# Kernel optimization log

Hardware: AMD Instinct MI355X
Metric: run time of the kernel (lower is better)

Reference implementation:

```python
import jax, jax.numpy as jnp
import numpy as np

B, L, H, E = 16, 4096, 8, 64
K = 64  # topk modes
SCALE = 1.0 / (512 * 512)  # 1/(in_channels*out_channels)


def setup_inputs() -> dict:
    key = jax.random.key(0)
    k1, k2, k3 = jax.random.split(key, 3)
    q = jax.random.normal(k1, (B, L, H, E), dtype=jnp.float32)
    k = jnp.zeros((B, L, H, E), jnp.float32)  # unused by module
    v = jnp.zeros((B, L, H, E), jnp.float32)  # unused by module
    mask = jnp.zeros((1,), jnp.int32)         # unused by module
    w_real = jax.random.uniform(k2, (K, H, E, E), dtype=jnp.float32) * SCALE
    w_imag = jax.random.uniform(k3, (K, H, E, E), dtype=jnp.float32) * SCALE
    return {"q": q, "k": k, "v": v, "w_real": w_real, "w_imag": w_imag, "mask": mask}


def reference(q, k, v, w_real, w_imag, mask):
    # x_ft: (B, F, H, Ein) complex64, F = L//2 + 1
    x_ft = jnp.fft.rfft(q.astype(jnp.float32), axis=1)
    F = x_ft.shape[1]
    kk = w_real.shape[0]
    # energy score per bin: sum |.|^2 over Ein, mean over batch, mean over heads
    e = (x_ft.real ** 2 + x_ft.imag ** 2).sum(-1)      # (B, F, H)
    score = e.mean(0).mean(-1)                          # (F,)
    score = score.at[0].set(-jnp.inf)                   # topk_exclude_dc=True
    _, idx = jax.lax.top_k(score, kk)                   # sorted desc by energy
    # gather selected modes: (B, K, H, Ein)
    x_sel = x_ft[:, idx]
    w = jax.lax.complex(w_real, w_imag)                 # (K, H, Ein, Eout)
    out_sel = jnp.einsum('bkhe,khef->bkhf', x_sel, w)   # per-head complex matmul
    # packed scatter: selected modes written into the first K bins of zero spectrum
    out_ft = jnp.zeros((x_ft.shape[0], F, x_ft.shape[2], w.shape[-1]), jnp.complex64)
    out_ft = out_ft.at[:, :kk].set(out_sel)
    # inverse FFT back to time domain, norm='backward' (default)
    return jnp.fft.irfft(out_ft, n=q.shape[1], axis=1)
```

## Files before the change

### kernel.cpp

```cpp
#include <hip/hip_runtime.h>


#define NTHREADS 256

__device__ inline void lds_barrier() {
    asm volatile("s_waitcnt lgkmcnt(0)" ::: "memory");
    __builtin_amdgcn_s_barrier();
}

#define ZI(i) ((i) ^ ((((i) >> 4) & 7) << 1))

__device__ inline float2 f2add(float2 a, float2 b) { return make_float2(a.x + b.x, a.y + b.y); }
__device__ inline float2 f2sub(float2 a, float2 b) { return make_float2(a.x - b.x, a.y - b.y); }
__device__ inline float2 cmulf(float2 a, float2 b) {
    return make_float2(__builtin_fmaf(a.x, b.x, -(a.y * b.y)),
                       __builtin_fmaf(a.x, b.y,  a.y * b.x));
}

__device__ inline void radix16(float2 x[16], float2 tA, float2 tB, float2 tC, float2 tD) {
#pragma unroll
    for (int q = 0; q < 8; ++q) {
        float2 v = cmulf(tA, x[2 * q + 1]);
        float2 u = x[2 * q];
        x[2 * q]     = f2add(u, v);
        x[2 * q + 1] = f2sub(u, v);
    }
    {
        float2 tB1 = make_float2(tB.y, -tB.x);
#pragma unroll
        for (int q = 0; q < 4; ++q) {
            {
                float2 v = cmulf(tB, x[4 * q + 2]);
                float2 u = x[4 * q];
                x[4 * q]     = f2add(u, v);
                x[4 * q + 2] = f2sub(u, v);
            }
            {
                float2 v = cmulf(tB1, x[4 * q + 3]);
                float2 u = x[4 * q + 1];
                x[4 * q + 1] = f2add(u, v);
                x[4 * q + 3] = f2sub(u, v);
            }
        }
    }
    {
        const float C = 0.70710678118654752f;
        float2 w0 = tC;
        float2 w1 = cmulf(tC, make_float2(C, -C));
        float2 w2 = make_float2(tC.y, -tC.x);
        float2 w3 = cmulf(tC, make_float2(-C, -C));
#pragma unroll
        for (int q = 0; q < 2; ++q) {
            float2 ws[4] = {w0, w1, w2, w3};
#pragma unroll
            for (int r = 0; r < 4; ++r) {
                float2 v = cmulf(ws[r], x[8 * q + r + 4]);
                float2 u = x[8 * q + r];
                x[8 * q + r]     = f2add(u, v);
                x[8 * q + r + 4] = f2sub(u, v);
            }
        }
    }
    {
        const float C  = 0.70710678118654752f;
        const float C1 = 0.92387953251128676f;
        const float S1 = 0.38268343236508977f;
        float2 wD[8];
        wD[0] = tD;
        wD[1] = cmulf(tD, make_float2(C1, -S1));
        wD[2] = cmulf(tD, make_float2(C, -C));
        wD[3] = cmulf(tD, make_float2(S1, -C1));
        wD[4] = make_float2(tD.y, -tD.x);
        wD[5] = cmulf(tD, make_float2(-S1, -C1));
        wD[6] = cmulf(tD, make_float2(-C, -C));
        wD[7] = cmulf(tD, make_float2(-C1, -S1));
#pragma unroll
        for (int r = 0; r < 8; ++r) {
            float2 v = cmulf(wD[r], x[r + 8]);
            float2 u = x[r];
            x[r]     = f2add(u, v);
            x[r + 8] = f2sub(u, v);
        }
    }
}

__global__ void k_tables(float2* __restrict__ trig, unsigned long long* __restrict__ score) {
    int k = blockIdx.x * blockDim.x + threadIdx.x;
    if (k < 4096) {
        double th = (6.283185307179586476925286766559 * (double)k) / 4096.0;
        trig[k] = make_float2((float)cos(th), (float)sin(th));
    }
    if (k < 2048) score[k] = 0ULL;
}

__global__ __launch_bounds__(256) void k_xpose(const float* __restrict__ q,
                                               float2* __restrict__ T) {
    __shared__ float tile[128][65];

    const int tid = threadIdx.x;
    const int bi  = blockIdx.x;
    const int b   = bi >> 8;
    const int h   = (bi >> 5) & 7;
    const int c5  = bi & 31;

    const float* qb = q + ((size_t)b * 4096 * 512) + (size_t)h * 64;
#pragma unroll
    for (int i = 0; i < 8; ++i) {
        const int f = tid + 256 * i;
        const int t = f >> 4, e4 = f & 15;
        const float4 v = *(const float4*)(qb + (size_t)(c5 + 32 * t) * 512 + e4 * 4);
        tile[t][e4 * 4 + 0] = v.x;
        tile[t][e4 * 4 + 1] = v.y;
        tile[t][e4 * 4 + 2] = v.z;
        tile[t][e4 * 4 + 3] = v.w;
    }
    lds_barrier();

    const int wave = tid >> 6, lane = tid & 63;
    const int rl  = __brev(lane) >> 26;
    const int r5c = __brev(c5) >> 27;
    for (int cc = wave; cc < 32; cc += 4) {
        const int eo = cc >> 2, p = cc & 3;
        const int col0 = eo * 8 + 2 * p;
        float2* dst = T + ((size_t)((b * 8 + h) * 8 + eo)) * 16384 + (size_t)p * 4096
                        + (size_t)r5c * 128;
        float4 o;
        o.x = tile[rl][col0];      o.y = tile[rl][col0 + 1];
        o.z = tile[rl + 64][col0]; o.w = tile[rl + 64][col0 + 1];
        *(float4*)(dst + 2 * lane) = o;
    }
}

__global__ __launch_bounds__(256) void k_fft(const float2* __restrict__ trig,
                                             float2* __restrict__ Xout,
                                             unsigned long long* __restrict__ score) {
    __shared__ float2 z[4096];
    __shared__ float2 ctw4[80];

    const int tid = threadIdx.x;
    const int bi  = blockIdx.x;

    if (tid < 64) {
        const int j = tid >> 2, qq = tid & 3;
        float2 a = trig[j << (7 - qq)];
        ctw4[5 * j + qq] = make_float2(a.x, -a.y);
    }

    float eaccr[8];
#pragma unroll
    for (int k = 0; k < 8; ++k) eaccr[k] = 0.f;

    const float2 ONE = make_float2(1.0f, 0.0f);
    const float2* base = Xout + (size_t)bi * 16384;

    float4 pre[8];
#pragma unroll
    for (int g = 0; g < 8; ++g) pre[g] = *(const float4*)(base + 16 * tid + 2 * g);
    lds_barrier();

    for (int p = 0; p < 4; ++p) {
        float2 x[16];
#pragma unroll
        for (int g = 0; g < 8; ++g) {
            x[2 * g]     = make_float2(pre[g].x, pre[g].y);
            x[2 * g + 1] = make_float2(pre[g].z, pre[g].w);
        }
        if (p < 3) {
            const float2* pn = base + (size_t)(p + 1) * 4096;
#pragma unroll
            for (int g = 0; g < 8; ++g) pre[g] = *(const float4*)(pn + 16 * tid + 2 * g);
        }

        radix16(x, ONE, ONE, ONE, ONE);
        {
            const int i0 = 16 * tid;
#pragma unroll
            for (int s = 0; s < 8; ++s) {
                *(float4*)&z[ZI(i0 + 2 * s)] = make_float4(x[2 * s].x, x[2 * s].y,
                                                           x[2 * s + 1].x, x[2 * s + 1].y);
            }
        }
        lds_barrier();

        {
            const int j = tid & 15;
            const int g = tid >> 4;
            const int i0 = (g << 8) + j;
            int ad[16];
#pragma unroll
            for (int k = 0; k < 16; ++k) ad[k] = ZI(i0 + 16 * k);
#pragma unroll
            for (int k = 0; k < 16; ++k) x[k] = z[ad[k]];
            const float2 tA = ctw4[5 * j + 0];
            const float2 tB = ctw4[5 * j + 1];
            const float2 tC = ctw4[5 * j + 2];
            const float2 tD = ctw4[5 * j + 3];
            radix16(x, tA, tB, tC, tD);
#pragma unroll
            for (int k = 0; k < 16; ++k) z[ad[k]] = x[k];
        }
        lds_barrier();

        {
            const int j = tid;
            int ad[16];
#pragma unroll
            for (int k = 0; k < 16; ++k) ad[k] = ZI(j + 256 * k);
#pragma unroll
            for (int k = 0; k < 16; ++k) x[k] = z[ad[k]];
            float2 a = trig[j << 3], b2 = trig[j << 2], c = trig[j << 1], d = trig[j];
            const float2 tA = make_float2(a.x, -a.y);
            const float2 tB = make_float2(b2.x, -b2.y);
            const float2 tC = make_float2(c.x, -c.y);
            const float2 tD = make_float2(d.x, -d.y);
            radix16(x, tA, tB, tC, tD);
#pragma unroll
            for (int k = 0; k < 16; ++k) z[ad[k]] = x[k];
        }
        lds_barrier();

        {
            const size_t s0 = (size_t)bi * 16384 + (size_t)p * 4096;
#pragma unroll
            for (int k = 0; k < 8; ++k) {
                const int t = tid + 256 * k;
                const int m = t + 1;
                float2 Za = z[ZI(m)];
                float2 Zb = z[ZI(4096 - m)];
                float Xr0 = 0.5f * (Za.x + Zb.x);
                float Xi0 = 0.5f * (Za.y - Zb.y);
                float Xr1 = 0.5f * (Za.y + Zb.y);
                float Xi1 = 0.5f * (Zb.x - Za.x);
                Xout[s0 + t]        = make_float2(Xr0, Xi0);
                Xout[s0 + 2048 + t] = make_float2(Xr1, Xi1);
                eaccr[k] += Xr0 * Xr0 + Xi0 * Xi0 + Xr1 * Xr1 + Xi1 * Xi1;
            }
        }
        lds_barrier();
    }

#pragma unroll
    for (int k = 0; k < 8; ++k) {
        unsigned long long v = (unsigned long long)llrintf(eaccr[k] * 1048576.0f);
        atomicAdd(&score[tid + 256 * k], v);
    }
}

__global__ __launch_bounds__(256) void k_topk(const unsigned long long* __restrict__ score,
                                              int* __restrict__ idx) {
    __shared__ unsigned long long s[2048];
    const int tid = threadIdx.x;
    for (int t = tid; t < 2048; t += 256) s[t] = score[t];
    __syncthreads();

    const int t = blockIdx.x * 256 + tid;
    const unsigned long long my = s[t];
    int rank = 0;
#pragma unroll 8
    for (int u = 0; u < 2048; ++u) {
        unsigned long long o = s[u];
        rank += (int)((o > my) || (o == my && u < t));
    }
    if (rank < 64) idx[rank] = t + 1;
}

__global__ __launch_bounds__(256) void k_proj(const float2* __restrict__ X,
                                              const float* __restrict__ wr,
                                              const float* __restrict__ wi,
                                              const int* __restrict__ idx,
                                              float2* __restrict__ Y) {
    __shared__ __align__(16) float2 xs[4 * 64];
    __shared__ float  wrs[64 * 64];
    __shared__ float  wis[64 * 64];

    const int tid = threadIdx.x;
    const int j  = blockIdx.x >> 5;
    const int h  = (blockIdx.x >> 2) & 7;
    const int bq = blockIdx.x & 3;
    const int m = idx[j];

    {
        const int bl = tid >> 6, e = tid & 63;
        xs[tid] = X[((size_t)(((bq * 4 + bl) * 8 + h) * 64 + e)) * 2048 + (size_t)(m - 1)];
    }
    const float* wrb = wr + ((size_t)(j * 8 + h)) * 4096;
    const float* wib = wi + ((size_t)(j * 8 + h)) * 4096;
#pragma unroll
    for (int i = 0; i < 16; ++i) {
        const int t = tid + 256 * i;
        wrs[t] = wrb[t];
        wis[t] = wib[t];
    }
    lds_barrier();

    const int bl = tid >> 6;
    const int f  = tid & 63;
    const float2* xrow = &xs[bl * 64];
    float yr = 0.f, yi = 0.f;
#pragma unroll
    for (int e = 0; e < 64; e += 4) {
        const float4 xa = *(const float4*)&xrow[e];
        const float4 xb = *(const float4*)&xrow[e + 2];
        const float2 xv[4] = {make_float2(xa.x, xa.y), make_float2(xa.z, xa.w),
                              make_float2(xb.x, xb.y), make_float2(xb.z, xb.w)};
#pragma unroll
        for (int d = 0; d < 4; ++d) {
            const float a = wrs[(e + d) * 64 + f], cc = wis[(e + d) * 64 + f];
            yr = __builtin_fmaf(xv[d].x, a, yr); yr = __builtin_fmaf(-xv[d].y, cc, yr);
            yi = __builtin_fmaf(xv[d].x, cc, yi); yi = __builtin_fmaf( xv[d].y, a, yi);
        }
    }
    const int b = bq * 4 + bl;
    Y[((size_t)b * 64 + j) * 512 + (size_t)(h * 64 + f)] = make_float2(yr, yi);
}

__global__ __launch_bounds__(256, 4) void k_synth(const float2* __restrict__ Y,
                                                  const float2* __restrict__ trig,
                                                  float* __restrict__ out) {
    __shared__ __align__(16) float2 ys[64][32];

    const int tid = threadIdx.x;
    const int bi  = blockIdx.x;
    const int b   = bi >> 8;
    const int hft = (bi >> 4) & 15;
    const int lt  = bi & 15;

    const float invN = 1.0f / 4096.0f;
    const float2* yb = Y + (size_t)b * 64 * 512 + (size_t)hft * 32;
    for (int t = tid; t < 64 * 32; t += NTHREADS) {
        int j = t >> 5, cc = t & 31;
        float2 y = yb[(size_t)j * 512 + cc];
        if (j == 0) ys[0][cc] = make_float2(y.x * invN, 0.0f);
        else        ys[j][cc] = make_float2(y.x * (2.0f * invN), y.y * (2.0f * invN));
    }
    lds_barrier();

    const int r = tid >> 3;
    const int c = tid & 7;
    const int l0 = lt * 64 + r * 2;

    float2 rot[2], w[2];
#pragma unroll
    for (int v = 0; v < 2; ++v) {
        w[v] = trig[(l0 + v) & 4095];
        rot[v] = make_float2(1.0f, 0.0f);
    }

    float F0[2][4], F1[2][4], F2[2][4], F3[2][4], H1[2][4], H3[2][4];
#pragma unroll
    for (int v = 0; v < 2; ++v)
#pragma unroll
        for (int u = 0; u < 4; ++u) {
            F0[v][u] = F1[v][u] = F2[v][u] = F3[v][u] = 0.0f;
            H1[v][u] = H3[v][u] = 0.0f;
        }

#define LOAD_YV(JROW)                                                        \
    float2 yv[4];                                                            \
    {                                                                        \
        const float4 ta = *(const float4*)&ys[(JROW)][c * 2];                \
        const float4 tb = *(const float4*)&ys[(JROW)][c * 2 + 16];           \
        yv[0] = make_float2(ta.x, ta.y); yv[1] = make_float2(ta.z, ta.w);    \
        yv[2] = make_float2(tb.x, tb.y); yv[3] = make_float2(tb.z, tb.w);    \
    }

    for (int j = 0; j < 64; j += 4) {
        {
            LOAD_YV(j)
#pragma unroll
            for (int v = 0; v < 2; ++v) {
                const float cx = rot[v].x, sx = rot[v].y;
#pragma unroll
                for (int u = 0; u < 4; ++u) {
                    float a = F0[v][u];
                    a = __builtin_fmaf(cx, yv[u].x, a);
                    a = __builtin_fmaf(-sx, yv[u].y, a);
                    F0[v][u] = a;
                }
                float nx = __builtin_fmaf(rot[v].x, w[v].x, -(rot[v].y * w[v].y));
                float ny = __builtin_fmaf(rot[v].x, w[v].y,  (rot[v].y * w[v].x));
                rot[v] = make_float2(nx, ny);
            }
        }
        {
            LOAD_YV(j + 1)
#pragma unroll
            for (int v = 0; v < 2; ++v) {
                const float cx = rot[v].x, sx = rot[v].y;
#pragma unroll
                for (int u = 0; u < 4; ++u) {
                    float a = F1[v][u], g = H1[v][u];
                    a = __builtin_fmaf(cx, yv[u].x, a);
                    a = __builtin_fmaf(-sx, yv[u].y, a);
                    g = __builtin_fmaf(sx, yv[u].x, g);
                    g = __builtin_fmaf(cx, yv[u].y, g);
                    F1[v][u] = a; H1[v][u] = g;
                }
                float nx = __builtin_fmaf(rot[v].x, w[v].x, -(rot[v].y * w[v].y));
                float ny = __builtin_fmaf(rot[v].x, w[v].y,  (rot[v].y * w[v].x));
                rot[v] = make_float2(nx, ny);
            }
        }
        {
            LOAD_YV(j + 2)
#pragma unroll
            for (int v = 0; v < 2; ++v) {
                const float cx = rot[v].x, sx = rot[v].y;
#pragma unroll
                for (int u = 0; u < 4; ++u) {
                    float a = F2[v][u];
                    a = __builtin_fmaf(cx, yv[u].x, a);
                    a = __builtin_fmaf(-sx, yv[u].y, a);
                    F2[v][u] = a;
                }
                float nx = __builtin_fmaf(rot[v].x, w[v].x, -(rot[v].y * w[v].y));
                float ny = __builtin_fmaf(rot[v].x, w[v].y,  (rot[v].y * w[v].x));
                rot[v] = make_float2(nx, ny);
            }
        }
        {
            LOAD_YV(j + 3)
#pragma unroll
            for (int v = 0; v < 2; ++v) {
                const float cx = rot[v].x, sx = rot[v].y;
#pragma unroll
                for (int u = 0; u < 4; ++u) {
                    float a = F3[v][u], g = H3[v][u];
                    a = __builtin_fmaf(cx, yv[u].x, a);
                    a = __builtin_fmaf(-sx, yv[u].y, a);
                    g = __builtin_fmaf(sx, yv[u].x, g);
                    g = __builtin_fmaf(cx, yv[u].y, g);
                    F3[v][u] = a; H3[v][u] = g;
                }
                float nx = __builtin_fmaf(rot[v].x, w[v].x, -(rot[v].y * w[v].y));
                float ny = __builtin_fmaf(rot[v].x, w[v].y,  (rot[v].y * w[v].x));
                rot[v] = make_float2(nx, ny);
            }
        }
    }
#undef LOAD_YV

#pragma unroll
    for (int v = 0; v < 2; ++v) {
        float* o0 = out + ((size_t)(b * 4096 + l0 + v)) * 512 + (size_t)hft * 32;
        float* o1 = o0 + (size_t)1024 * 512;
        float* o2 = o0 + (size_t)2048 * 512;
        float* o3 = o0 + (size_t)3072 * 512;
#pragma unroll
        for (int k = 0; k < 2; ++k) {
            float2 s0, s1, s2, s3;
#pragma unroll
            for (int d = 0; d < 2; ++d) {
                const int u = 2 * k + d;
                const float p = F0[v][u] + F2[v][u];
                const float m = F0[v][u] - F2[v][u];
                const float q = F1[v][u] + F3[v][u];
                const float hh = H3[v][u] - H1[v][u];
                ((float*)&s0)[d] = p + q;
                ((float*)&s2)[d] = p - q;
                ((float*)&s1)[d] = m + hh;
                ((float*)&s3)[d] = m - hh;
            }
            *(float2*)(o0 + k * 16 + c * 2) = s0;
            *(float2*)(o1 + k * 16 + c * 2) = s1;
            *(float2*)(o2 + k * 16 + c * 2) = s2;
            *(float2*)(o3 + k * 16 + c * 2) = s3;
        }
    }
}

extern "C" void kernel_launch(void* const* d_in, const int* in_sizes, int n_in,
                              void* d_out, int out_size, void* d_ws, size_t ws_size,
                              hipStream_t stream) {
    const float* q  = (const float*)d_in[0];
    const float* wr = (const float*)d_in[3];
    const float* wi = (const float*)d_in[4];

    char* ws = (char*)d_ws;
    float2*             trig  = (float2*)(ws + 0);
    unsigned long long* score = (unsigned long long*)(ws + 32768);
    int*                idx   = (int*)(ws + 49152);
    float2*             Y     = (float2*)(ws + 65536);

    float2* Xs = (float2*)d_out;

    k_tables<<<16, 256, 0, stream>>>(trig, score);
    k_xpose<<<4096, 256, 0, stream>>>(q, Xs);
    k_fft<<<1024, 256, 0, stream>>>(trig, Xs, score);
    k_topk<<<8, 256, 0, stream>>>(score, idx);
    k_proj<<<2048, 256, 0, stream>>>(Xs, wr, wi, idx, Y);
    k_synth<<<4096, 256, 0, stream>>>(Y, trig, (float*)d_out);
}
```

Measured before the change: 241.9 us.

## Recast inverse DFT synthesis as fp16 MFMA GEMM against precomputed twiddle matrix

Replaces the scalar FMA synthesis kernel, which walked rotating twiddles with a radix-4 split, with a GEMM. A precomputed fp16 cos/-sin matrix (4096x128) is multiplied by an fp16 packed spectrum (real and imaginary parts of 64 modes per channel) using 16x16x32 f16 MFMA instructions. The projection kernel now writes that transposed half-precision spectrum directly, halving the DC term. This moves the dominant synthesis work onto matrix cores but lowers precision to fp16 inputs and adds a kernel that builds the twiddle matrix on every call.

```diff
diff --git a/kernel.cpp b/kernel.cpp
--- a/kernel.cpp
+++ b/kernel.cpp
@@ -2,6 +2,9 @@
 
 
 #define NTHREADS 256
+
+typedef _Float16 f16x8 __attribute__((ext_vector_type(8)));
+typedef float    f32x4 __attribute__((ext_vector_type(4)));
 
 __device__ inline void lds_barrier() {
     asm volatile("s_waitcnt lgkmcnt(0)" ::: "memory");
@@ -93,6 +96,14 @@
     if (k < 2048) score[k] = 0ULL;
 }
 
+__global__ __launch_bounds__(256) void k_af(const float2* __restrict__ trig,
+                                            _Float16* __restrict__ Af) {
+    const int gid = blockIdx.x * 256 + threadIdx.x;
+    const int l = gid >> 7, k = gid & 127;
+    float v = (k < 64) ? trig[(k * l) & 4095].x : -trig[((k - 64) * l) & 4095].y;
+    Af[gid] = (_Float16)v;
+}
+
 __global__ __launch_bounds__(256) void k_xpose(const float* __restrict__ q,
                                                float2* __restrict__ T) {
     __shared__ float tile[128][65];
@@ -268,7 +279,7 @@
                                               const float* __restrict__ wr,
                                               const float* __restrict__ wi,
                                               const int* __restrict__ idx,
-                                              float2* __restrict__ Y) {
+                                              _Float16* __restrict__ Yt) {
     __shared__ __align__(16) float2 xs[4 * 64];
     __shared__ float  wrs[64 * 64];
     __shared__ float  wis[64 * 64];
@@ -310,161 +321,63 @@
             yi = __builtin_fmaf(xv[d].x, cc, yi); yi = __builtin_fmaf( xv[d].y, a, yi);
         }
     }
-    const int b = bq * 4 + bl;
-    Y[((size_t)b * 64 + j) * 512 + (size_t)(h * 64 + f)] = make_float2(yr, yi);
-}
-
-__global__ __launch_bounds__(256, 4) void k_synth(const float2* __restrict__ Y,
-                                                  const float2* __restrict__ trig,
-                                                  float* __restrict__ out) {
-    __shared__ __align__(16) float2 ys[64][32];
-
-    const int tid = threadIdx.x;
-    const int bi  = blockIdx.x;
-    const int b   = bi >> 8;
-    const int hft = (bi >> 4) & 15;
-    const int lt  = bi & 15;
-
-    const float invN = 1.0f / 4096.0f;
-    const float2* yb = Y + (size_t)b * 64 * 512 + (size_t)hft * 32;
-    for (int t = tid; t < 64 * 32; t += NTHREADS) {
-        int j = t >> 5, cc = t & 31;
-        float2 y = yb[(size_t)j * 512 + cc];
-        if (j == 0) ys[0][cc] = make_float2(y.x * invN, 0.0f);
-        else        ys[j][cc] = make_float2(y.x * (2.0f * invN), y.y * (2.0f * invN));
-    }
-    lds_barrier();
-
-    const int r = tid >> 3;
-    const int c = tid & 7;
-    const int l0 = lt * 64 + r * 2;
-
-    float2 rot[2], w[2];
-#pragma unroll
-    for (int v = 0; v < 2; ++v) {
-        w[v] = trig[(l0 + v) & 4095];
-        rot[v] = make_float2(1.0f, 0.0f);
-    }
-
-    float F0[2][4], F1[2][4], F2[2][4], F3[2][4], H1[2][4], H3[2][4];
-#pragma unroll
-    for (int v = 0; v < 2; ++v)
-#pragma unroll
-        for (int u = 0; u < 4; ++u) {
-            F0[v][u] = F1[v][u] = F2[v][u] = F3[v][u] = 0.0f;
-            H1[v][u] = H3[v][u] = 0.0f;
-        }
-
-#define LOAD_YV(JROW)                                                        \
-    float2 yv[4];                                                            \
-    {                                                                        \
-        const float4 ta = *(const float4*)&ys[(JROW)][c * 2];                \
-        const float4 tb = *(const float4*)&ys[(JROW)][c * 2 + 16];           \
-        yv[0] = make_float2(ta.x, ta.y); yv[1] = make_float2(ta.z, ta.w);    \
-        yv[2] = make_float2(tb.x, tb.y); yv[3] = make_float2(tb.z, tb.w);    \
-    }
-
-    for (int j = 0; j < 64; j += 4) {
-        {
-            LOAD_YV(j)
-#pragma unroll
-            for (int v = 0; v < 2; ++v) {
-                const float cx = rot[v].x, sx = rot[v].y;
-#pragma unroll
-                for (int u = 0; u < 4; ++u) {
-                    float a = F0[v][u];
-                    a = __builtin_fmaf(cx, yv[u].x, a);
-                    a = __builtin_fmaf(-sx, yv[u].y, a);
-                    F0[v][u] = a;
-                }
-                float nx = __builtin_fmaf(rot[v].x, w[v].x, -(rot[v].y * w[v].y));
-                float ny = __builtin_fmaf(rot[v].x, w[v].y,  (rot[v].y * w[v].x));
-                rot[v] = make_float2(nx, ny);
-            }
-        }
-        {
-            LOAD_YV(j + 1)
-#pragma unroll
-            for (int v = 0; v < 2; ++v) {
-                const float cx = rot[v].x, sx = rot[v].y;
-#pragma unroll
-                for (int u = 0; u < 4; ++u) {
-                    float a = F1[v][u], g = H1[v][u];
-                    a = __builtin_fmaf(cx, yv[u].x, a);
-                    a = __builtin_fmaf(-sx, yv[u].y, a);
-                    g = __builtin_fmaf(sx, yv[u].x, g);
-                    g = __builtin_fmaf(cx, yv[u].y, g);
-                    F1[v][u] = a; H1[v][u] = g;
-                }
-                float nx = __builtin_fmaf(rot[v].x, w[v].x, -(rot[v].y * w[v].y));
-                float ny = __builtin_fmaf(rot[v].x, w[v].y,  (rot[v].y * w[v].x));
-                rot[v] = make_float2(nx, ny);
-            }
-        }
-        {
-            LOAD_YV(j + 2)
-#pragma unroll
-            for (int v = 0; v < 2; ++v) {
-                const float cx = rot[v].x, sx = rot[v].y;
-#pragma unroll
-                for (int u = 0; u < 4; ++u) {
-                    float a = F2[v][u];
-                    a = __builtin_fmaf(cx, yv[u].x, a);
-                    a = __builtin_fmaf(-sx, yv[u].y, a);
-                    F2[v][u] = a;
-                }
-                float nx = __builtin_fmaf(rot[v].x, w[v].x, -(rot[v].y * w[v].y));
-                float ny = __builtin_fmaf(rot[v].x, w[v].y,  (rot[v].y * w[v].x));
-                rot[v] = make_float2(nx, ny);
-            }
-        }
-        {
-            LOAD_YV(j + 3)
-#pragma unroll
-            for (int v = 0; v < 2; ++v) {
-                const float cx = rot[v].x, sx = rot[v].y;
-#pragma unroll
-                for (int u = 0; u < 4; ++u) {
-                    float a = F3[v][u], g = H3[v][u];
-                    a = __builtin_fmaf(cx, yv[u].x, a);
-                    a = __builtin_fmaf(-sx, yv[u].y, a);
-                    g = __builtin_fmaf(sx, yv[u].x, g);
-                    g = __builtin_fmaf(cx, yv[u].y, g);
-                    F3[v][u] = a; H3[v][u] = g;
-                }
-                float nx = __builtin_fmaf(rot[v].x, w[v].x, -(rot[v].y * w[v].y));
-                float ny = __builtin_fmaf(rot[v].x, w[v].y,  (rot[v].y * w[v].x));
-                rot[v] = make_float2(nx, ny);
-            }
-        }
-    }
-#undef LOAD_YV
-
-#pragma unroll
-    for (int v = 0; v < 2; ++v) {
-        float* o0 = out + ((size_t)(b * 4096 + l0 + v)) * 512 + (size_t)hft * 32;
-        float* o1 = o0 + (size_t)1024 * 512;
-        float* o2 = o0 + (size_t)2048 * 512;
-        float* o3 = o0 + (size_t)3072 * 512;
-#pragma unroll
-        for (int k = 0; k < 2; ++k) {
-            float2 s0, s1, s2, s3;
-#pragma unroll
-            for (int d = 0; d < 2; ++d) {
-                const int u = 2 * k + d;
-                const float p = F0[v][u] + F2[v][u];
-                const float m = F0[v][u] - F2[v][u];
-                const float q = F1[v][u] + F3[v][u];
-                const float hh = H3[v][u] - H1[v][u];
-                ((float*)&s0)[d] = p + q;
-                ((float*)&s2)[d] = p - q;
-                ((float*)&s1)[d] = m + hh;
-                ((float*)&s3)[d] = m - hh;
-            }
-            *(float2*)(o0 + k * 16 + c * 2) = s0;
-            *(float2*)(o1 + k * 16 + c * 2) = s1;
-            *(float2*)(o2 + k * 16 + c * 2) = s2;
-            *(float2*)(o3 + k * 16 + c * 2) = s3;
+    const int b  = bq * 4 + bl;
+    const int hf = h * 64 + f;
+    _Float16* yt = Yt + ((size_t)b * 512 + (size_t)hf) * 128;
+    yt[j]      = (_Float16)(j == 0 ? 0.5f * yr : yr);
+    yt[64 + j] = (_Float16)yi;
+}
+
+__global__ __launch_bounds__(256) void k_synth(const _Float16* __restrict__ Af,
+                                               const _Float16* __restrict__ Yt,
+                                               float* __restrict__ out) {
+    const int tid  = threadIdx.x;
+    const int wv   = tid >> 6;
+    const int lane = tid & 63;
+    const int bi   = blockIdx.x;
+    const int b    = bi >> 8;
+    const int ng   = (bi >> 6) & 3;
+    const int lt   = bi & 63;
+
+    const int l0 = lt * 64;
+    const int n0 = ng * 128 + wv * 32;
+
+    const int row = lane & 15;
+    const int kb  = lane >> 4;
+
+    f32x4 acc[4][2] = {};
+
+    const _Float16* Ab = Af + (size_t)l0 * 128;
+    const _Float16* Bb = Yt + (size_t)b * 512 * 128 + (size_t)n0 * 128;
+
+#pragma unroll
+    for (int k0 = 0; k0 < 128; k0 += 32) {
+        f16x8 a[4], bf[2];
+#pragma unroll
+        for (int mt = 0; mt < 4; ++mt)
+            a[mt] = *(const f16x8*)(Ab + (size_t)(mt * 16 + row) * 128 + k0 + kb * 8);
+#pragma unroll
+        for (int nt = 0; nt < 2; ++nt)
+            bf[nt] = *(const f16x8*)(Bb + (size_t)(nt * 16 + row) * 128 + k0 + kb * 8);
+#pragma unroll
+        for (int mt = 0; mt < 4; ++mt)
+#pragma unroll
+            for (int nt = 0; nt < 2; ++nt)
+                acc[mt][nt] = __builtin_amdgcn_mfma_f32_16x16x32_f16(a[mt], bf[nt],
+                                                                     acc[mt][nt], 0, 0, 0);
+    }
+
+    const float s = 2.0f / 4096.0f;
+#pragma unroll
+    for (int mt = 0; mt < 4; ++mt) {
+#pragma unroll
+        for (int nt = 0; nt < 2; ++nt) {
+            const int col = n0 + nt * 16 + row;
+#pragma unroll
+            for (int r = 0; r < 4; ++r) {
+                const int mrow = mt * 16 + kb * 4 + r;
+                out[((size_t)(b * 4096 + l0 + mrow)) * 512 + col] = acc[mt][nt][r] * s;
+            }
         }
     }
 }
@@ -480,14 +393,16 @@
     float2*             trig  = (float2*)(ws + 0);
     unsigned long long* score = (unsigned long long*)(ws + 32768);
     int*                idx   = (int*)(ws + 49152);
-    float2*             Y     = (float2*)(ws + 65536);
+    _Float16*           Af    = (_Float16*)(ws + 65536);
+    _Float16*           Yt    = (_Float16*)(ws + 65536 + 1048576);
 
     float2* Xs = (float2*)d_out;
 
     k_tables<<<16, 256, 0, stream>>>(trig, score);
+    k_af<<<2048, 256, 0, stream>>>(trig, Af);
     k_xpose<<<4096, 256, 0, stream>>>(q, Xs);
     k_fft<<<1024, 256, 0, stream>>>(trig, Xs, score);
     k_topk<<<8, 256, 0, stream>>>(score, idx);
-    k_proj<<<2048, 256, 0, stream>>>(Xs, wr, wi, idx, Y);
-    k_synth<<<4096, 256, 0, stream>>>(Y, trig, (float*)d_out);
-}
+    k_proj<<<2048, 256, 0, stream>>>(Xs, wr, wi, idx, Yt);
+    k_synth<<<4096, 256, 0, stream>>>(Af, Yt, (float*)d_out);
+}
```

Result: faster. 234.7 us (-3.0%).
